# Kernel tuning notes

Measured on AMD Instinct MI355X. Metric: run time of the kernel, lower is better.

Reference implementation:

```python
import jax, jax.numpy as jnp
import numpy as np

DIM = 192; D_STATE = 16; D_CONV = 4; EXPAND = 2
D_INNER = EXPAND * DIM          # 384
DT_RANK = -(-DIM // 16)         # ceil(192/16) = 12
BSZ, T, H, W = 1, 16, 64, 64


def setup_inputs() -> dict:
    key = jax.random.key(0)
    ks = jax.random.split(key, 10)
    s = 0.02
    return {
        "x": jax.random.normal(ks[0], (BSZ, DIM, T, H, W), jnp.float32),
        "ln1_g": jnp.ones((DIM,), jnp.float32),
        "ln1_b": jnp.zeros((DIM,), jnp.float32),
        "ln2_g": jnp.ones((DIM,), jnp.float32),
        "ln2_b": jnp.zeros((DIM,), jnp.float32),
        "W_in": jax.random.normal(ks[1], (2 * D_INNER, DIM), jnp.float32) * s,
        "conv_w": jax.random.normal(ks[2], (D_INNER, D_CONV), jnp.float32) * 0.3,
        "conv_b": jnp.zeros((D_INNER,), jnp.float32),
        "W_xp": jax.random.normal(ks[3], (DT_RANK + 2 * D_STATE, D_INNER), jnp.float32) * s,
        "W_dt": jax.random.normal(ks[4], (D_INNER, DT_RANK), jnp.float32) * 0.1,
        "b_dt": jax.random.normal(ks[5], (D_INNER,), jnp.float32) * 0.1 - 4.0,
        "A_log": jnp.log(jnp.broadcast_to(jnp.arange(1, D_STATE + 1, dtype=jnp.float32), (D_INNER, D_STATE))),
        "D": jnp.ones((D_INNER,), jnp.float32),
        "W_out": jax.random.normal(ks[6], (DIM, D_INNER), jnp.float32) * s,
    }


def _layer_norm(x, g, b, eps=1e-5):
    m = x.mean(-1, keepdims=True)
    v = ((x - m) ** 2).mean(-1, keepdims=True)
    return (x - m) * jax.lax.rsqrt(v + eps) * g + b


def _mamba(tokens, W_in, conv_w, conv_b, W_xp, W_dt, b_dt, A_log, D, W_out):
    B, L, _ = tokens.shape
    xz = tokens @ W_in.T                      # (B, L, 2*d_inner)
    xc, z = jnp.split(xz, 2, axis=-1)
    # causal depthwise conv1d along L
    xin = xc.transpose(0, 2, 1)               # (B, d_inner, L)
    xconv = jax.lax.conv_general_dilated(
        xin, conv_w[:, None, :], (1,), [(D_CONV - 1, 0)],
        dimension_numbers=("NCH", "OIH", "NCH"), feature_group_count=D_INNER)
    xconv = xconv + conv_b[None, :, None]
    xs = jax.nn.silu(xconv.transpose(0, 2, 1))  # (B, L, d_inner)
    x_dbl = xs @ W_xp.T                        # (B, L, dt_rank + 2*d_state)
    dt, Bm, Cm = jnp.split(x_dbl, [DT_RANK, DT_RANK + D_STATE], axis=-1)
    dt = jax.nn.softplus(dt @ W_dt.T + b_dt)   # (B, L, d_inner)
    A = -jnp.exp(A_log)                        # (d_inner, d_state)
    dA = jnp.exp(dt[..., None] * A)            # (B, L, d_inner, d_state)
    dBx = dt[..., None] * Bm[:, :, None, :] * xs[..., None]

    def step(h, inp):
        dA_t, dBx_t, C_t = inp
        h = dA_t * h + dBx_t                   # (B, d_inner, d_state)
        return h, jnp.einsum("bds,bs->bd", h, C_t)

    h0 = jnp.zeros((B, D_INNER, D_STATE), tokens.dtype)
    _, ys = jax.lax.scan(step, h0, (dA.transpose(1, 0, 2, 3),
                                    dBx.transpose(1, 0, 2, 3),
                                    Cm.transpose(1, 0, 2)))
    y = ys.transpose(1, 0, 2) + xs * D         # (B, L, d_inner)
    y = y * jax.nn.silu(z)
    return y @ W_out.T                          # (B, L, dim)


def reference(x, ln1_g, ln1_b, ln2_g, ln2_b, W_in, conv_w, conv_b,
              W_xp, W_dt, b_dt, A_log, D, W_out):
    B, C, T_, H_, W_ = x.shape
    Hs, Ws = H_ // 4, W_ // 4
    # avg_pool3d kernel=(1,4,4) stride=(1,4,4)
    x_ds = x.reshape(B, C, T_, Hs, 4, Ws, 4).mean((4, 6))
    tokens = x_ds.reshape(B, C, T_ * Hs * Ws).transpose(0, 2, 1)  # (B, L, C)
    y = _layer_norm(tokens, ln1_g, ln1_b)
    y = _mamba(y, W_in, conv_w, conv_b, W_xp, W_dt, b_dt, A_log, D, W_out)
    out = _layer_norm(tokens + y, ln2_g, ln2_b)                    # (B, L, C)
    out5 = out.transpose(0, 2, 1).reshape(B, C, T_, Hs, Ws)
    pooled = out5.mean((3, 4))                                     # (B, C, T)
    mag = jnp.abs(jnp.fft.rfft(pooled, axis=2))
    weight = jax.nn.sigmoid(mag[:, :, 1:8].mean(-1))               # (B, C)
    out5 = out5 * weight[:, :, None, None, None]
    up = jax.image.resize(out5, (B, C, T_, H_, W_), method="trilinear")
    return up * jax.nn.sigmoid(x)
```

## Files before the change

### kernel.cpp

```cpp
#include <hip/hip_runtime.h>
#include <math.h>

#define DIMC 192
#define DI   384
#define DS   16
#define LTOK 4096
#define NCH  256
#define CLEN 16
#define NLANE (DI*DS)
#define L2E  1.4426950408889634f
#define LN2  0.6931471805599453f

typedef __attribute__((ext_vector_type(8))) short    bf16x8;
typedef __attribute__((ext_vector_type(8))) unsigned short u16x8;
typedef __attribute__((ext_vector_type(4))) float    f32x4;

__device__ __forceinline__ float EXP2(float x) { return __builtin_amdgcn_exp2f(x); }
__device__ __forceinline__ float RCP(float x)  { return __builtin_amdgcn_rcpf(x); }
__device__ __forceinline__ float LOG2(float x) { return __builtin_amdgcn_logf(x); }

__device__ __forceinline__ float sigmoidf_(float x) { return RCP(1.f + EXP2(-x * L2E)); }
__device__ __forceinline__ float siluf_(float x)    { return x * RCP(1.f + EXP2(-x * L2E)); }
__device__ __forceinline__ unsigned short f2bf(float f) {
    unsigned int u = __float_as_uint(f);
    u += 0x7FFFu + ((u >> 16) & 1u);
    return (unsigned short)(u >> 16);
}
__device__ __forceinline__ float bf2f(unsigned short b) {
    return __uint_as_float(((unsigned int)b) << 16);
}

__global__ __launch_bounds__(256) void poolln_kernel(const float* __restrict__ x,
                                                     const float* __restrict__ g,
                                                     const float* __restrict__ bb,
                                                     const float* __restrict__ W_in,
                                                     const float* __restrict__ W_out,
                                                     const float* __restrict__ W_xp,
                                                     const float* __restrict__ A_log,
                                                     float* __restrict__ tokens,
                                                     unsigned short* __restrict__ ytok,
                                                     unsigned short* __restrict__ W_in_bf,
                                                     unsigned short* __restrict__ W_out_bf,
                                                     unsigned short* __restrict__ W_xp_pad,
                                                     float* __restrict__ A2pre) {
    int blk = blockIdx.x;
    int tid = threadIdx.x;
    if (blk >= 256) {
        int id = (blk - 256) * 256 + tid;
        for (int i = id; i < 768 * 192; i += 8192) W_in_bf[i] = f2bf(W_in[i]);
        for (int i = id; i < 192 * 384; i += 8192) W_out_bf[i] = f2bf(W_out[i]);
        for (int i = id; i < 64 * 384; i += 8192) {
            int row = i / 384;
            W_xp_pad[i] = (row < 44) ? f2bf(W_xp[i]) : (unsigned short)0;
        }
        for (int i = id; i < NLANE; i += 8192) A2pre[i] = -expf(A_log[i]) * L2E;
        return;
    }
    int t = blk >> 4, hs = blk & 15;
    int grp = tid >> 4, ws = tid & 15;
    __shared__ float P[16 * 196];
    __shared__ float ms[16], rs[16];
    #pragma unroll
    for (int k = 0; k < 12; ++k) {
        int c = grp + (k << 4);
        const float* base = x + ((size_t)(c * 16 + t) * 64 + hs * 4) * 64 + ws * 4;
        float s = 0.f;
        #pragma unroll
        for (int i = 0; i < 4; ++i) {
            float4 v = *(const float4*)(base + i * 64);
            s += v.x + v.y + v.z + v.w;
        }
        P[ws * 196 + c] = s * 0.0625f;
    }
    __syncthreads();
    float s1 = 0.f, s2 = 0.f;
    #pragma unroll
    for (int k = 0; k < 12; ++k) {
        float v = P[grp * 196 + ws + 16 * k];
        s1 += v; s2 += v * v;
    }
    s1 += __shfl_xor(s1, 1); s2 += __shfl_xor(s2, 1);
    s1 += __shfl_xor(s1, 2); s2 += __shfl_xor(s2, 2);
    s1 += __shfl_xor(s1, 4); s2 += __shfl_xor(s2, 4);
    s1 += __shfl_xor(s1, 8); s2 += __shfl_xor(s2, 8);
    if (ws == 0) {
        float m = s1 * (1.f / 192.f);
        ms[grp] = m;
        rs[grp] = rsqrtf(s2 * (1.f / 192.f) - m * m + 1e-5f);
    }
    __syncthreads();
    int l0 = t * 256 + hs * 16;
    for (int e = tid; e < 16 * 192; e += 256) {
        int w2 = e / 192, c = e - w2 * 192;
        float v = P[w2 * 196 + c];
        float val = (v - ms[w2]) * rs[w2] * g[c] + bb[c];
        tokens[(size_t)(l0 + w2) * DIMC + c] = v;
        ytok[(size_t)(l0 + w2) * DIMC + c] = f2bf(val);
    }
}

template<int K>
__global__ __launch_bounds__(256) void gemm_mfma(const unsigned short* __restrict__ A,
                                                 const unsigned short* __restrict__ Wb,
                                                 float* __restrict__ Cout,
                                                 int N) {
    constexpr int KT = 192;
    constexpr int KP = KT + 8;
    __shared__ unsigned short As[64 * KP];
    __shared__ unsigned short Bs[64 * KP];
    int bm = blockIdx.y * 64;
    int bn = blockIdx.x * 64;
    int tid = threadIdx.x;
    int lane = tid & 63, w = tid >> 6;
    int wr = w >> 1, wc = w & 1;
    int r16 = lane & 15, h = lane >> 4;
    f32x4 acc[2][2] = {};
    for (int kt = 0; kt < K; kt += KT) {
        for (int c = tid; c < 64 * (KT / 8); c += 256) {
            int row = c / (KT / 8), col = (c % (KT / 8)) * 8;
            *(u16x8*)&As[row * KP + col] = *(const u16x8*)(A + (size_t)(bm + row) * K + kt + col);
            *(u16x8*)&Bs[row * KP + col] = *(const u16x8*)(Wb + (size_t)(bn + row) * K + kt + col);
        }
        __syncthreads();
        #pragma unroll
        for (int k0 = 0; k0 < KT; k0 += 32) {
            bf16x8 a0 = *(const bf16x8*)&As[(wr * 32 + r16)      * KP + k0 + 8 * h];
            bf16x8 a1 = *(const bf16x8*)&As[(wr * 32 + 16 + r16) * KP + k0 + 8 * h];
            bf16x8 b0 = *(const bf16x8*)&Bs[(wc * 32 + r16)      * KP + k0 + 8 * h];
            bf16x8 b1 = *(const bf16x8*)&Bs[(wc * 32 + 16 + r16) * KP + k0 + 8 * h];
            acc[0][0] = __builtin_amdgcn_mfma_f32_16x16x32_bf16(a0, b0, acc[0][0], 0, 0, 0);
            acc[0][1] = __builtin_amdgcn_mfma_f32_16x16x32_bf16(a0, b1, acc[0][1], 0, 0, 0);
            acc[1][0] = __builtin_amdgcn_mfma_f32_16x16x32_bf16(a1, b0, acc[1][0], 0, 0, 0);
            acc[1][1] = __builtin_amdgcn_mfma_f32_16x16x32_bf16(a1, b1, acc[1][1], 0, 0, 0);
        }
        __syncthreads();
    }
    #pragma unroll
    for (int fm = 0; fm < 2; ++fm)
        #pragma unroll
        for (int fn = 0; fn < 2; ++fn)
            #pragma unroll
            for (int i = 0; i < 4; ++i) {
                int r = bm + wr * 32 + fm * 16 + h * 4 + i;
                int cc = bn + wc * 32 + fn * 16 + r16;
                Cout[(size_t)r * N + cc] = acc[fm][fn][i];
            }
}

__global__ __launch_bounds__(256) void convxdbl(const float* __restrict__ xz,
                                                const float* __restrict__ conv_w,
                                                const float* __restrict__ conv_b,
                                                const unsigned short* __restrict__ Wxp,
                                                unsigned short* __restrict__ xsb,
                                                float* __restrict__ x_dbl) {
    int l0 = blockIdx.x * 16;
    int tid = threadIdx.x;
    __shared__ unsigned short As[16 * 392];
    __shared__ float xd[16 * 64];
    for (int e = tid * 2; e < 16 * 384; e += 512) {
        int row = e / 384, d = e - row * 384;
        int l = l0 + row;
        float ax = conv_b[d], ay = conv_b[d + 1];
        #pragma unroll
        for (int k = 0; k < 4; ++k) {
            int ll = l - 3 + k;
            if (ll >= 0) {
                float2 v = *(const float2*)(xz + (size_t)ll * 768 + d);
                ax = fmaf(conv_w[d * 4 + k],       v.x, ax);
                ay = fmaf(conv_w[(d + 1) * 4 + k], v.y, ay);
            }
        }
        ushort2 b2;
        b2.x = f2bf(siluf_(ax));
        b2.y = f2bf(siluf_(ay));
        *(ushort2*)&As[row * 392 + d] = b2;
        *(ushort2*)(xsb + (size_t)l * 384 + d) = b2;
    }
    __syncthreads();
    int lane = tid & 63, w = tid >> 6;
    int r16 = lane & 15, hh = lane >> 4;
    f32x4 acc = {};
    #pragma unroll
    for (int k0 = 0; k0 < 384; k0 += 32) {
        bf16x8 a = *(const bf16x8*)&As[r16 * 392 + k0 + 8 * hh];
        bf16x8 b = *(const bf16x8*)(Wxp + (size_t)(w * 16 + r16) * 384 + k0 + 8 * hh);
        acc = __builtin_amdgcn_mfma_f32_16x16x32_bf16(a, b, acc, 0, 0, 0);
    }
    #pragma unroll
    for (int i = 0; i < 4; ++i) xd[(hh * 4 + i) * 64 + w * 16 + r16] = acc[i];
    __syncthreads();
    {
        int e = tid * 4;
        int row = e >> 6, col = e & 63;
        *(float4*)(x_dbl + (size_t)(l0 + row) * 64 + col) = *(const float4*)&xd[e];
    }
}

__global__ __launch_bounds__(256) void scan1(const float* __restrict__ x_dbl,
                                             const unsigned short* __restrict__ xsb,
                                             const float* __restrict__ W_dt,
                                             const float* __restrict__ b_dt,
                                             const float* __restrict__ A2pre,
                                             float* __restrict__ chA,
                                             float* __restrict__ chB,
                                             float* __restrict__ Dloc,
                                             unsigned short* __restrict__ yloc) {
    int tid = threadIdx.x;
    int dg = blockIdx.x;
    int c  = blockIdx.y;
    __shared__ float xdblS[16 * 48];
    __shared__ float wdtS[64 * 13];
    __shared__ float dtS[16][64];
    __shared__ unsigned short xsS[16][64];
    for (int i = tid; i < 768; i += 256) {
        int row = i / 48, col = i - row * 48;
        xdblS[i] = x_dbl[(size_t)(c * 16 + row) * 64 + col];
    }
    for (int i = tid; i < 768; i += 256) {
        int dl_ = i / 12, r = i - dl_ * 12;
        wdtS[dl_ * 13 + r] = W_dt[(size_t)dg * 768 + i];
    }
    for (int i = tid; i < 1024; i += 256) {
        int row = i >> 6, dl_ = i & 63;
        xsS[row][dl_] = xsb[(size_t)(c * 16 + row) * 384 + dg * 64 + dl_];
    }
    __syncthreads();
    {
        int dl_ = tid & 63;
        float bd = b_dt[dg * 64 + dl_];
        #pragma unroll
        for (int i2 = 0; i2 < 4; ++i2) {
            int row = (tid >> 6) + 4 * i2;
            float s = bd;
            #pragma unroll
            for (int r = 0; r < 12; ++r)
                s = fmaf(xdblS[row * 48 + r], wdtS[dl_ * 13 + r], s);
            dtS[row][dl_] = (s > 20.f) ? s : LOG2(1.f + EXP2(s * L2E)) * LN2;
        }
    }
    __syncthreads();
    int sq = tid & 3, dl = tid >> 2;
    int d = dg * 64 + dl;
    float4 a4 = *(const float4*)(A2pre + (size_t)d * DS + sq * 4);
    float A2[4] = {a4.x, a4.y, a4.z, a4.w};
    float h[4] = {};
    float dts = 0.f;
    #pragma unroll
    for (int i = 0; i < CLEN; ++i) {
        int l = c * CLEN + i;
        float dtv = dtS[i][dl];
        float xv  = bf2f(xsS[i][dl]);
        float dtx = dtv * xv;
        dts += dtv;
        float y = 0.f;
        #pragma unroll
        for (int u = 0; u < 4; ++u) {
            float a = EXP2(dtv * A2[u]);
            h[u] = fmaf(a, h[u], dtx * xdblS[i * 48 + 12 + sq * 4 + u]);
            y = fmaf(h[u], xdblS[i * 48 + 28 + sq * 4 + u], y);
        }
        y += __shfl_xor(y, 1);
        y += __shfl_xor(y, 2);
        if (sq == 0) {
            yloc[(size_t)l * DI + d] = f2bf(y);
            Dloc[(size_t)l * DI + d] = dts;
        }
    }
    size_t base = (size_t)c * NLANE + d * DS + sq * 4;
    float4 pa, pb;
    pa.x = EXP2(dts * A2[0]); pa.y = EXP2(dts * A2[1]);
    pa.z = EXP2(dts * A2[2]); pa.w = EXP2(dts * A2[3]);
    pb.x = h[0]; pb.y = h[1]; pb.z = h[2]; pb.w = h[3];
    *(float4*)&chA[base] = pa;
    *(float4*)&chB[base] = pb;
}

__global__ __launch_bounds__(256) void scan2p(const float* __restrict__ chA,
                                              const float* __restrict__ chB,
                                              float* __restrict__ hst) {
    int tid = threadIdx.x;
    int ll = tid & 15;
    int g  = tid >> 4;
    int lane = blockIdx.x * 16 + ll;
    float a[16], b[16];
    #pragma unroll
    for (int i = 0; i < 16; ++i) {
        int c = g * 16 + i;
        a[i] = chA[(size_t)c * NLANE + lane];
        b[i] = chB[(size_t)c * NLANE + lane];
    }
    float Ath = 1.f, Bth = 0.f;
    #pragma unroll
    for (int i = 0; i < 16; ++i) {
        Bth = fmaf(a[i], Bth, b[i]);
        Ath *= a[i];
    }
    __shared__ float sA[16][17], sB[16][17];
    sA[g][ll] = Ath; sB[g][ll] = Bth;
    __syncthreads();
    #pragma unroll
    for (int step = 1; step < 16; step <<= 1) {
        float pA = 1.f, pB = 0.f;
        if (g >= step) { pA = sA[g - step][ll]; pB = sB[g - step][ll]; }
        __syncthreads();
        if (g >= step) {
            float cA = sA[g][ll], cB = sB[g][ll];
            sA[g][ll] = cA * pA;
            sB[g][ll] = fmaf(cA, pB, cB);
        }
        __syncthreads();
    }
    float h = (g == 0) ? 0.f : sB[g - 1][ll];
    #pragma unroll
    for (int i = 0; i < 16; ++i) {
        int c = g * 16 + i;
        hst[(size_t)c * NLANE + lane] = h;
        h = fmaf(a[i], h, b[i]);
    }
}

__global__ __launch_bounds__(256) void scan3fix(const float* __restrict__ hst,
                                                const float* __restrict__ Dloc,
                                                const float* __restrict__ x_dbl,
                                                const float* __restrict__ A2pre,
                                                const unsigned short* __restrict__ xsb,
                                                const float* __restrict__ xz,
                                                const float* __restrict__ Dvec,
                                                unsigned short* __restrict__ ybuf) {
    int dg = blockIdx.x;
    int c  = blockIdx.y;
    int tid = threadIdx.x;
    int ll = tid >> 4, dl = tid & 15;
    int d = dg * 16 + dl;
    int l = c * 16 + ll;
    __shared__ float hpS[16][17];
    __shared__ float A2S[16][17];
    __shared__ float CsS[256];
    {
        int dd = tid >> 4, ss = tid & 15;
        hpS[dd][ss] = hst[(size_t)c * NLANE + dg * 256 + tid];
        A2S[dd][ss] = A2pre[(size_t)dg * 256 + tid];
        CsS[tid]    = x_dbl[(size_t)(c * 16 + dd) * 64 + 28 + ss];
    }
    __syncthreads();
    float Dl = Dloc[(size_t)l * DI + d];
    float y  = bf2f(ybuf[(size_t)l * DI + d]);
    float xv = bf2f(xsb[(size_t)l * DI + d]);
    float z  = xz[(size_t)l * 768 + 384 + d];
    #pragma unroll
    for (int s = 0; s < 16; ++s) {
        float e = EXP2(A2S[dl][s] * Dl);
        y = fmaf(CsS[ll * 16 + s] * e, hpS[dl][s], y);
    }
    float val = (y + xv * Dvec[d]) * siluf_(z);
    ybuf[(size_t)l * DI + d] = f2bf(val);
}

__global__ __launch_bounds__(256) void gemmln(const unsigned short* __restrict__ A,
                                              const unsigned short* __restrict__ Wb,
                                              const float* __restrict__ tokens,
                                              const float* __restrict__ g,
                                              const float* __restrict__ bb,
                                              float* __restrict__ o5) {
    constexpr int K = 384, KT = 96, KP = KT + 8;
    __shared__ unsigned short As[16 * KP];
    __shared__ unsigned short Bs[192 * KP];
    __shared__ float P[16 * 193];
    __shared__ float ms[16], rs[16];
    int bm = blockIdx.x * 16;
    int tid = threadIdx.x;
    int lane = tid & 63, w = tid >> 6;
    int r16 = lane & 15, hh = lane >> 4;
    f32x4 acc[3] = {};
    for (int kt = 0; kt < K; kt += KT) {
        if (tid < 192) {
            int row = tid / 12, col = (tid % 12) * 8;
            *(u16x8*)&As[row * KP + col] = *(const u16x8*)(A + (size_t)(bm + row) * K + kt + col);
        }
        for (int cc = tid; cc < 192 * 12; cc += 256) {
            int row = cc / 12, col = (cc % 12) * 8;
            *(u16x8*)&Bs[row * KP + col] = *(const u16x8*)(Wb + (size_t)row * K + kt + col);
        }
        __syncthreads();
        #pragma unroll
        for (int k0 = 0; k0 < KT; k0 += 32) {
            bf16x8 a = *(const bf16x8*)&As[r16 * KP + k0 + 8 * hh];
            #pragma unroll
            for (int j = 0; j < 3; ++j) {
                bf16x8 b = *(const bf16x8*)&Bs[((w * 3 + j) * 16 + r16) * KP + k0 + 8 * hh];
                acc[j] = __builtin_amdgcn_mfma_f32_16x16x32_bf16(a, b, acc[j], 0, 0, 0);
            }
        }
        __syncthreads();
    }
    for (int e = tid; e < 16 * 192; e += 256) {
        int row = e / 192, col = e - row * 192;
        P[row * 193 + col] = tokens[(size_t)(bm + row) * DIMC + col];
    }
    __syncthreads();
    #pragma unroll
    for (int j = 0; j < 3; ++j)
        #pragma unroll
        for (int i = 0; i < 4; ++i)
            P[(hh * 4 + i) * 193 + (w * 3 + j) * 16 + r16] += acc[j][i];
    __syncthreads();
    {
        int tk = tid >> 4, q = tid & 15;
        float s1 = 0.f, s2 = 0.f;
        #pragma unroll
        for (int u = 0; u < 12; ++u) {
            float v = P[tk * 193 + q * 12 + u];
            s1 += v; s2 += v * v;
        }
        s1 += __shfl_xor(s1, 1); s2 += __shfl_xor(s2, 1);
        s1 += __shfl_xor(s1, 2); s2 += __shfl_xor(s2, 2);
        s1 += __shfl_xor(s1, 4); s2 += __shfl_xor(s2, 4);
        s1 += __shfl_xor(s1, 8); s2 += __shfl_xor(s2, 8);
        if (q == 0) {
            float m = s1 * (1.f / 192.f);
            ms[tk] = m;
            rs[tk] = rsqrtf(s2 * (1.f / 192.f) - m * m + 1e-5f);
        }
    }
    __syncthreads();
    int t = bm >> 8;
    int sp0 = bm & 255;
    for (int e = tid; e < 16 * 192; e += 256) {
        int cch = e >> 4, row = e & 15;
        float val = (P[row * 193 + cch] - ms[row]) * rs[row] * g[cch] + bb[cch];
        o5[(size_t)cch * 4096 + t * 256 + sp0 + row] = val;
    }
}

__global__ __launch_bounds__(256) void upfft(const float* __restrict__ o5,
                                             const float* __restrict__ x,
                                             float* __restrict__ out) {
    int blk = blockIdx.x;
    int c = blk >> 4, t = blk & 15;
    int tid = threadIdx.x;
    __shared__ float pl[256];
    __shared__ float pooled[16];
    __shared__ float mag[8];
    __shared__ float wgt_s;
    int wv = tid >> 6, lane = tid & 63;
    #pragma unroll
    for (int rr = 0; rr < 4; ++rr) {
        int r = wv * 4 + rr;
        float s = 0.f;
        #pragma unroll
        for (int u = 0; u < 4; ++u) {
            float v = o5[(size_t)c * 4096 + r * 256 + lane + u * 64];
            s += v;
            if (r == t) pl[lane + u * 64] = v;
        }
        s += __shfl_xor(s, 1); s += __shfl_xor(s, 2); s += __shfl_xor(s, 4);
        s += __shfl_xor(s, 8); s += __shfl_xor(s, 16); s += __shfl_xor(s, 32);
        if (lane == 0) pooled[r] = s * (1.f / 256.f);
    }
    __syncthreads();
    if (tid >= 1 && tid <= 7) {
        int k = tid;
        float re = 0.f, im = 0.f;
        for (int tt = 0; tt < 16; ++tt) {
            float ang = -0.39269908169872414f * (float)(k * tt);
            re = fmaf(pooled[tt], cosf(ang), re);
            im = fmaf(pooled[tt], sinf(ang), im);
        }
        mag[k] = sqrtf(re * re + im * im);
    }
    __syncthreads();
    if (tid == 0) {
        float m = 0.f;
        for (int k = 1; k <= 7; ++k) m += mag[k];
        wgt_s = sigmoidf_(m * (1.f / 7.f));
    }
    __syncthreads();
    float wc = wgt_s;
    size_t planeoff = (size_t)blk * 4096;
    #pragma unroll
    for (int p = 0; p < 4; ++p) {
        int px4 = p * 256 + tid;
        int k = px4 & 15;
        int hrow = px4 >> 4;
        float sh = hrow * 0.25f - 0.375f;
        int h0 = (int)floorf(sh); float fh = sh - (float)h0;
        int h0c = min(max(h0, 0), 15), h1c = min(max(h0 + 1, 0), 15);
        int cm = max(k - 1, 0), cp = min(k + 1, 15);
        float r0m = pl[h0c * 16 + cm], r00 = pl[h0c * 16 + k], r0p = pl[h0c * 16 + cp];
        float r1m = pl[h1c * 16 + cm], r10 = pl[h1c * 16 + k], r1p = pl[h1c * 16 + cp];
        float gh = 1.f - fh;
        float vm = r0m * gh + r1m * fh;
        float v0 = r00 * gh + r10 * fh;
        float vp = r0p * gh + r1p * fh;
        size_t off = planeoff + (size_t)px4 * 4;
        float4 xv = *(const float4*)(x + off);
        float4 o;
        o.x = (vm * 0.375f + v0 * 0.625f) * wc * sigmoidf_(xv.x);
        o.y = (vm * 0.125f + v0 * 0.875f) * wc * sigmoidf_(xv.y);
        o.z = (v0 * 0.875f + vp * 0.125f) * wc * sigmoidf_(xv.z);
        o.w = (v0 * 0.625f + vp * 0.375f) * wc * sigmoidf_(xv.w);
        *(float4*)(out + off) = o;
    }
}

extern "C" void kernel_launch(void* const* d_in, const int* in_sizes, int n_in,
                              void* d_out, int out_size, void* d_ws, size_t ws_size,
                              hipStream_t stream) {
    const float* x      = (const float*)d_in[0];
    const float* ln1_g  = (const float*)d_in[1];
    const float* ln1_b  = (const float*)d_in[2];
    const float* ln2_g  = (const float*)d_in[3];
    const float* ln2_b  = (const float*)d_in[4];
    const float* W_in   = (const float*)d_in[5];
    const float* conv_w = (const float*)d_in[6];
    const float* conv_b = (const float*)d_in[7];
    const float* W_xp   = (const float*)d_in[8];
    const float* W_dt   = (const float*)d_in[9];
    const float* b_dt   = (const float*)d_in[10];
    const float* A_log  = (const float*)d_in[11];
    const float* Dvec   = (const float*)d_in[12];
    const float* W_out  = (const float*)d_in[13];
    float* out = (float*)d_out;

    float* ws = (float*)d_ws;
    float* tokens = ws;  ws += (size_t)LTOK * DIMC;
    float* xz     = ws;  ws += (size_t)LTOK * 768;
    float* x_dbl  = ws;  ws += (size_t)LTOK * 64;
    float* chA    = ws;  ws += (size_t)NLANE * NCH;
    float* chB    = ws;  ws += (size_t)NLANE * NCH;
    float* hst    = ws;  ws += (size_t)NLANE * NCH;
    float* Dloc   = ws;  ws += (size_t)LTOK * DI;
    float* o5     = ws;  ws += (size_t)DIMC * LTOK;
    float* A2pre  = ws;  ws += NLANE;
    unsigned short* ytok     = (unsigned short*)ws;  ws += (size_t)LTOK * DIMC / 2;
    unsigned short* ybuf     = (unsigned short*)ws;  ws += (size_t)LTOK * DI / 2;
    unsigned short* xsb      = (unsigned short*)ws;  ws += (size_t)LTOK * DI / 2;
    unsigned short* W_in_bf  = (unsigned short*)ws;  ws += (size_t)768 * 192 / 2;
    unsigned short* W_out_bf = (unsigned short*)ws;  ws += (size_t)192 * 384 / 2;
    unsigned short* W_xp_pad = (unsigned short*)ws;  ws += (size_t)64 * 384 / 2;

    poolln_kernel<<<288, 256, 0, stream>>>(x, ln1_g, ln1_b, W_in, W_out, W_xp, A_log,
                                           tokens, ytok, W_in_bf, W_out_bf, W_xp_pad, A2pre);
    gemm_mfma<192><<<dim3(12, 64), 256, 0, stream>>>(ytok, W_in_bf, xz, 768);
    convxdbl<<<256, 256, 0, stream>>>(xz, conv_w, conv_b, W_xp_pad, xsb, x_dbl);
    scan1<<<dim3(6, NCH), 256, 0, stream>>>(x_dbl, xsb, W_dt, b_dt, A2pre, chA, chB, Dloc, ybuf);
    scan2p<<<NLANE / 16, 256, 0, stream>>>(chA, chB, hst);
    scan3fix<<<dim3(24, NCH), 256, 0, stream>>>(hst, Dloc, x_dbl, A2pre, xsb, xz, Dvec, ybuf);
    gemmln<<<256, 256, 0, stream>>>(ybuf, W_out_bf, tokens, ln2_g, ln2_b, o5);
    upfft<<<3072, 256, 0, stream>>>(o5, x, out);
}
```

Before: 125.5 us.

## Fuse scan fix-up into output GEMM+LN and emit bf16 x/silu(z) from input GEMM

The input projection GEMM now writes bf16 xc and a precomputed bf16 silu(z) instead of a float32 xz buffer, which halves that intermediate traffic. The scan fix-up kernel is merged into the W_out GEMM + LayerNorm kernel (512 threads per 16-token chunk), so the gated y stays in shared memory and is never written to or read back from global memory. This drops one launch but gives the fused kernel only 256 blocks, each doing serial work over 12 d-groups. It also switches the FFT to fast __sinf/__cosf, and storing z and xc in bf16 adds some rounding.

New measurement: 110.9 us. 1.13x faster.

```diff
diff --git a/kernel.cpp b/kernel.cpp
--- a/kernel.cpp
+++ b/kernel.cpp
@@ -99,13 +99,11 @@
     }
 }
 
-template<int K>
-__global__ __launch_bounds__(256) void gemm_mfma(const unsigned short* __restrict__ A,
-                                                 const unsigned short* __restrict__ Wb,
-                                                 float* __restrict__ Cout,
-                                                 int N) {
-    constexpr int KT = 192;
-    constexpr int KP = KT + 8;
+__global__ __launch_bounds__(256) void gemm_in(const unsigned short* __restrict__ A,
+                                               const unsigned short* __restrict__ Wb,
+                                               unsigned short* __restrict__ xcb,
+                                               unsigned short* __restrict__ zsb) {
+    constexpr int K = 192, KP = K + 8;
     __shared__ unsigned short As[64 * KP];
     __shared__ unsigned short Bs[64 * KP];
     int bm = blockIdx.y * 64;
@@ -114,27 +112,25 @@
     int lane = tid & 63, w = tid >> 6;
     int wr = w >> 1, wc = w & 1;
     int r16 = lane & 15, h = lane >> 4;
+    for (int c = tid; c < 64 * (K / 8); c += 256) {
+        int row = c / (K / 8), col = (c % (K / 8)) * 8;
+        *(u16x8*)&As[row * KP + col] = *(const u16x8*)(A + (size_t)(bm + row) * K + col);
+        *(u16x8*)&Bs[row * KP + col] = *(const u16x8*)(Wb + (size_t)(bn + row) * K + col);
+    }
+    __syncthreads();
     f32x4 acc[2][2] = {};
-    for (int kt = 0; kt < K; kt += KT) {
-        for (int c = tid; c < 64 * (KT / 8); c += 256) {
-            int row = c / (KT / 8), col = (c % (KT / 8)) * 8;
-            *(u16x8*)&As[row * KP + col] = *(const u16x8*)(A + (size_t)(bm + row) * K + kt + col);
-            *(u16x8*)&Bs[row * KP + col] = *(const u16x8*)(Wb + (size_t)(bn + row) * K + kt + col);
-        }
-        __syncthreads();
-        #pragma unroll
-        for (int k0 = 0; k0 < KT; k0 += 32) {
-            bf16x8 a0 = *(const bf16x8*)&As[(wr * 32 + r16)      * KP + k0 + 8 * h];
-            bf16x8 a1 = *(const bf16x8*)&As[(wr * 32 + 16 + r16) * KP + k0 + 8 * h];
-            bf16x8 b0 = *(const bf16x8*)&Bs[(wc * 32 + r16)      * KP + k0 + 8 * h];
-            bf16x8 b1 = *(const bf16x8*)&Bs[(wc * 32 + 16 + r16) * KP + k0 + 8 * h];
-            acc[0][0] = __builtin_amdgcn_mfma_f32_16x16x32_bf16(a0, b0, acc[0][0], 0, 0, 0);
-            acc[0][1] = __builtin_amdgcn_mfma_f32_16x16x32_bf16(a0, b1, acc[0][1], 0, 0, 0);
-            acc[1][0] = __builtin_amdgcn_mfma_f32_16x16x32_bf16(a1, b0, acc[1][0], 0, 0, 0);
-            acc[1][1] = __builtin_amdgcn_mfma_f32_16x16x32_bf16(a1, b1, acc[1][1], 0, 0, 0);
-        }
-        __syncthreads();
-    }
+    #pragma unroll
+    for (int k0 = 0; k0 < K; k0 += 32) {
+        bf16x8 a0 = *(const bf16x8*)&As[(wr * 32 + r16)      * KP + k0 + 8 * h];
+        bf16x8 a1 = *(const bf16x8*)&As[(wr * 32 + 16 + r16) * KP + k0 + 8 * h];
+        bf16x8 b0 = *(const bf16x8*)&Bs[(wc * 32 + r16)      * KP + k0 + 8 * h];
+        bf16x8 b1 = *(const bf16x8*)&Bs[(wc * 32 + 16 + r16) * KP + k0 + 8 * h];
+        acc[0][0] = __builtin_amdgcn_mfma_f32_16x16x32_bf16(a0, b0, acc[0][0], 0, 0, 0);
+        acc[0][1] = __builtin_amdgcn_mfma_f32_16x16x32_bf16(a0, b1, acc[0][1], 0, 0, 0);
+        acc[1][0] = __builtin_amdgcn_mfma_f32_16x16x32_bf16(a1, b0, acc[1][0], 0, 0, 0);
+        acc[1][1] = __builtin_amdgcn_mfma_f32_16x16x32_bf16(a1, b1, acc[1][1], 0, 0, 0);
+    }
+    bool isz = (bn >= 384);
     #pragma unroll
     for (int fm = 0; fm < 2; ++fm)
         #pragma unroll
@@ -143,11 +139,13 @@
             for (int i = 0; i < 4; ++i) {
                 int r = bm + wr * 32 + fm * 16 + h * 4 + i;
                 int cc = bn + wc * 32 + fn * 16 + r16;
-                Cout[(size_t)r * N + cc] = acc[fm][fn][i];
+                float v = acc[fm][fn][i];
+                if (isz) zsb[(size_t)r * DI + (cc - 384)] = f2bf(siluf_(v));
+                else     xcb[(size_t)r * DI + cc]         = f2bf(v);
             }
 }
 
-__global__ __launch_bounds__(256) void convxdbl(const float* __restrict__ xz,
+__global__ __launch_bounds__(256) void convxdbl(const unsigned short* __restrict__ xcb,
                                                 const float* __restrict__ conv_w,
                                                 const float* __restrict__ conv_b,
                                                 const unsigned short* __restrict__ Wxp,
@@ -165,9 +163,9 @@
         for (int k = 0; k < 4; ++k) {
             int ll = l - 3 + k;
             if (ll >= 0) {
-                float2 v = *(const float2*)(xz + (size_t)ll * 768 + d);
-                ax = fmaf(conv_w[d * 4 + k],       v.x, ax);
-                ay = fmaf(conv_w[(d + 1) * 4 + k], v.y, ay);
+                ushort2 u = *(const ushort2*)(xcb + (size_t)ll * DI + d);
+                ax = fmaf(conv_w[d * 4 + k],       bf2f(u.x), ax);
+                ay = fmaf(conv_w[(d + 1) * 4 + k], bf2f(u.y), ay);
             }
         }
         ushort2 b2;
@@ -319,103 +317,100 @@
     }
 }
 
-__global__ __launch_bounds__(256) void scan3fix(const float* __restrict__ hst,
-                                                const float* __restrict__ Dloc,
-                                                const float* __restrict__ x_dbl,
-                                                const float* __restrict__ A2pre,
-                                                const unsigned short* __restrict__ xsb,
-                                                const float* __restrict__ xz,
-                                                const float* __restrict__ Dvec,
-                                                unsigned short* __restrict__ ybuf) {
-    int dg = blockIdx.x;
-    int c  = blockIdx.y;
-    int tid = threadIdx.x;
-    int ll = tid >> 4, dl = tid & 15;
-    int d = dg * 16 + dl;
+__global__ __launch_bounds__(512) void gemmscanln(const float* __restrict__ hst,
+                                                  const float* __restrict__ Dloc,
+                                                  const float* __restrict__ x_dbl,
+                                                  const float* __restrict__ A2pre,
+                                                  const unsigned short* __restrict__ yloc,
+                                                  const unsigned short* __restrict__ xsb,
+                                                  const unsigned short* __restrict__ zsb,
+                                                  const float* __restrict__ Dvec,
+                                                  const unsigned short* __restrict__ Wb,
+                                                  const float* __restrict__ tokens,
+                                                  const float* __restrict__ g,
+                                                  const float* __restrict__ bb,
+                                                  float* __restrict__ o5) {
+    constexpr int K = 384, KT = 96, KP = KT + 8;
+    __shared__ unsigned short ybufS[16 * 392];
+    __shared__ char smem2[192 * KP * 2];
+    unsigned short* Bs = (unsigned short*)smem2;
+    float* P = (float*)smem2;
+    __shared__ float hpS[2][16 * 17];
+    __shared__ float A2S[2][16 * 17];
+    __shared__ float CsS[256];
+    __shared__ float ms[16], rs[16];
+    int c = blockIdx.x;
+    int tid = threadIdx.x;
+    int half = tid >> 8, t8 = tid & 255;
+    int ll = t8 >> 4, sl = t8 & 15;
+    if (tid < 256) CsS[tid] = x_dbl[(size_t)(c * 16 + (tid >> 4)) * 64 + 28 + (tid & 15)];
     int l = c * 16 + ll;
-    __shared__ float hpS[16][17];
-    __shared__ float A2S[16][17];
-    __shared__ float CsS[256];
-    {
-        int dd = tid >> 4, ss = tid & 15;
-        hpS[dd][ss] = hst[(size_t)c * NLANE + dg * 256 + tid];
-        A2S[dd][ss] = A2pre[(size_t)dg * 256 + tid];
-        CsS[tid]    = x_dbl[(size_t)(c * 16 + dd) * 64 + 28 + ss];
-    }
-    __syncthreads();
-    float Dl = Dloc[(size_t)l * DI + d];
-    float y  = bf2f(ybuf[(size_t)l * DI + d]);
-    float xv = bf2f(xsb[(size_t)l * DI + d]);
-    float z  = xz[(size_t)l * 768 + 384 + d];
-    #pragma unroll
-    for (int s = 0; s < 16; ++s) {
-        float e = EXP2(A2S[dl][s] * Dl);
-        y = fmaf(CsS[ll * 16 + s] * e, hpS[dl][s], y);
-    }
-    float val = (y + xv * Dvec[d]) * siluf_(z);
-    ybuf[(size_t)l * DI + d] = f2bf(val);
-}
-
-__global__ __launch_bounds__(256) void gemmln(const unsigned short* __restrict__ A,
-                                              const unsigned short* __restrict__ Wb,
-                                              const float* __restrict__ tokens,
-                                              const float* __restrict__ g,
-                                              const float* __restrict__ bb,
-                                              float* __restrict__ o5) {
-    constexpr int K = 384, KT = 96, KP = KT + 8;
-    __shared__ unsigned short As[16 * KP];
-    __shared__ unsigned short Bs[192 * KP];
-    __shared__ float P[16 * 193];
-    __shared__ float ms[16], rs[16];
-    int bm = blockIdx.x * 16;
-    int tid = threadIdx.x;
+    for (int dgi = 0; dgi < 12; ++dgi) {
+        int dg = dgi * 2 + half;
+        hpS[half][ll * 17 + sl] = hst[(size_t)c * NLANE + dg * 256 + t8];
+        A2S[half][ll * 17 + sl] = A2pre[(size_t)dg * 256 + t8];
+        __syncthreads();
+        int d = dg * 16 + sl;
+        float Dl = Dloc[(size_t)l * DI + d];
+        float y  = bf2f(yloc[(size_t)l * DI + d]);
+        float xv = bf2f(xsb[(size_t)l * DI + d]);
+        float zs = bf2f(zsb[(size_t)l * DI + d]);
+        #pragma unroll
+        for (int s = 0; s < 16; ++s) {
+            float e = EXP2(A2S[half][sl * 17 + s] * Dl);
+            y = fmaf(CsS[ll * 16 + s] * e, hpS[half][sl * 17 + s], y);
+        }
+        float val = (y + xv * Dvec[d]) * zs;
+        ybufS[ll * 392 + d] = f2bf(val);
+        __syncthreads();
+    }
     int lane = tid & 63, w = tid >> 6;
     int r16 = lane & 15, hh = lane >> 4;
-    f32x4 acc[3] = {};
+    f32x4 acc0 = {}, acc1 = {};
     for (int kt = 0; kt < K; kt += KT) {
-        if (tid < 192) {
-            int row = tid / 12, col = (tid % 12) * 8;
-            *(u16x8*)&As[row * KP + col] = *(const u16x8*)(A + (size_t)(bm + row) * K + kt + col);
-        }
-        for (int cc = tid; cc < 192 * 12; cc += 256) {
-            int row = cc / 12, col = (cc % 12) * 8;
+        for (int cc2 = tid; cc2 < 192 * 12; cc2 += 512) {
+            int row = cc2 / 12, col = (cc2 % 12) * 8;
             *(u16x8*)&Bs[row * KP + col] = *(const u16x8*)(Wb + (size_t)row * K + kt + col);
         }
         __syncthreads();
         #pragma unroll
         for (int k0 = 0; k0 < KT; k0 += 32) {
-            bf16x8 a = *(const bf16x8*)&As[r16 * KP + k0 + 8 * hh];
-            #pragma unroll
-            for (int j = 0; j < 3; ++j) {
-                bf16x8 b = *(const bf16x8*)&Bs[((w * 3 + j) * 16 + r16) * KP + k0 + 8 * hh];
-                acc[j] = __builtin_amdgcn_mfma_f32_16x16x32_bf16(a, b, acc[j], 0, 0, 0);
+            bf16x8 a = *(const bf16x8*)&ybufS[r16 * 392 + kt + k0 + 8 * hh];
+            bf16x8 b0 = *(const bf16x8*)&Bs[(w * 16 + r16) * KP + k0 + 8 * hh];
+            acc0 = __builtin_amdgcn_mfma_f32_16x16x32_bf16(a, b0, acc0, 0, 0, 0);
+            if (w < 4) {
+                bf16x8 b1 = *(const bf16x8*)&Bs[((8 + w) * 16 + r16) * KP + k0 + 8 * hh];
+                acc1 = __builtin_amdgcn_mfma_f32_16x16x32_bf16(a, b1, acc1, 0, 0, 0);
             }
         }
         __syncthreads();
     }
-    for (int e = tid; e < 16 * 192; e += 256) {
+    for (int e = tid; e < 16 * 192; e += 512) {
         int row = e / 192, col = e - row * 192;
-        P[row * 193 + col] = tokens[(size_t)(bm + row) * DIMC + col];
-    }
-    __syncthreads();
-    #pragma unroll
-    for (int j = 0; j < 3; ++j)
+        P[row * 193 + col] = tokens[(size_t)(c * 16 + row) * DIMC + col];
+    }
+    __syncthreads();
+    #pragma unroll
+    for (int i = 0; i < 4; ++i)
+        P[(hh * 4 + i) * 193 + w * 16 + r16] += acc0[i];
+    if (w < 4)
         #pragma unroll
         for (int i = 0; i < 4; ++i)
-            P[(hh * 4 + i) * 193 + (w * 3 + j) * 16 + r16] += acc[j][i];
+            P[(hh * 4 + i) * 193 + (8 + w) * 16 + r16] += acc1[i];
     __syncthreads();
     {
-        int tk = tid >> 4, q = tid & 15;
+        int tk = tid >> 5, q = tid & 31;
         float s1 = 0.f, s2 = 0.f;
         #pragma unroll
-        for (int u = 0; u < 12; ++u) {
-            float v = P[tk * 193 + q * 12 + u];
+        for (int u = 0; u < 6; ++u) {
+            float v = P[tk * 193 + q * 6 + u];
             s1 += v; s2 += v * v;
         }
-        s1 += __shfl_xor(s1, 1); s2 += __shfl_xor(s2, 1);
-        s1 += __shfl_xor(s1, 2); s2 += __shfl_xor(s2, 2);
-        s1 += __shfl_xor(s1, 4); s2 += __shfl_xor(s2, 4);
-        s1 += __shfl_xor(s1, 8); s2 += __shfl_xor(s2, 8);
+        s1 += __shfl_xor(s1, 1);  s2 += __shfl_xor(s2, 1);
+        s1 += __shfl_xor(s1, 2);  s2 += __shfl_xor(s2, 2);
+        s1 += __shfl_xor(s1, 4);  s2 += __shfl_xor(s2, 4);
+        s1 += __shfl_xor(s1, 8);  s2 += __shfl_xor(s2, 8);
+        s1 += __shfl_xor(s1, 16); s2 += __shfl_xor(s2, 16);
         if (q == 0) {
             float m = s1 * (1.f / 192.f);
             ms[tk] = m;
@@ -423,9 +418,9 @@
         }
     }
     __syncthreads();
-    int t = bm >> 8;
-    int sp0 = bm & 255;
-    for (int e = tid; e < 16 * 192; e += 256) {
+    int t = c >> 4;
+    int sp0 = (c * 16) & 255;
+    for (int e = tid; e < 16 * 192; e += 512) {
         int cch = e >> 4, row = e & 15;
         float val = (P[row * 193 + cch] - ms[row]) * rs[row] * g[cch] + bb[cch];
         o5[(size_t)cch * 4096 + t * 256 + sp0 + row] = val;
@@ -463,8 +458,8 @@
         float re = 0.f, im = 0.f;
         for (int tt = 0; tt < 16; ++tt) {
             float ang = -0.39269908169872414f * (float)(k * tt);
-            re = fmaf(pooled[tt], cosf(ang), re);
-            im = fmaf(pooled[tt], sinf(ang), im);
+            re = fmaf(pooled[tt], __cosf(ang), re);
+            im = fmaf(pooled[tt], __sinf(ang), im);
         }
         mag[k] = sqrtf(re * re + im * im);
     }
@@ -524,7 +519,6 @@
 
     float* ws = (float*)d_ws;
     float* tokens = ws;  ws += (size_t)LTOK * DIMC;
-    float* xz     = ws;  ws += (size_t)LTOK * 768;
     float* x_dbl  = ws;  ws += (size_t)LTOK * 64;
     float* chA    = ws;  ws += (size_t)NLANE * NCH;
     float* chB    = ws;  ws += (size_t)NLANE * NCH;
@@ -533,19 +527,21 @@
     float* o5     = ws;  ws += (size_t)DIMC * LTOK;
     float* A2pre  = ws;  ws += NLANE;
     unsigned short* ytok     = (unsigned short*)ws;  ws += (size_t)LTOK * DIMC / 2;
-    unsigned short* ybuf     = (unsigned short*)ws;  ws += (size_t)LTOK * DI / 2;
+    unsigned short* yloc     = (unsigned short*)ws;  ws += (size_t)LTOK * DI / 2;
     unsigned short* xsb      = (unsigned short*)ws;  ws += (size_t)LTOK * DI / 2;
+    unsigned short* xcb      = (unsigned short*)ws;  ws += (size_t)LTOK * DI / 2;
+    unsigned short* zsb      = (unsigned short*)ws;  ws += (size_t)LTOK * DI / 2;
     unsigned short* W_in_bf  = (unsigned short*)ws;  ws += (size_t)768 * 192 / 2;
     unsigned short* W_out_bf = (unsigned short*)ws;  ws += (size_t)192 * 384 / 2;
     unsigned short* W_xp_pad = (unsigned short*)ws;  ws += (size_t)64 * 384 / 2;
 
     poolln_kernel<<<288, 256, 0, stream>>>(x, ln1_g, ln1_b, W_in, W_out, W_xp, A_log,
                                            tokens, ytok, W_in_bf, W_out_bf, W_xp_pad, A2pre);
-    gemm_mfma<192><<<dim3(12, 64), 256, 0, stream>>>(ytok, W_in_bf, xz, 768);
-    convxdbl<<<256, 256, 0, stream>>>(xz, conv_w, conv_b, W_xp_pad, xsb, x_dbl);
-    scan1<<<dim3(6, NCH), 256, 0, stream>>>(x_dbl, xsb, W_dt, b_dt, A2pre, chA, chB, Dloc, ybuf);
+    gemm_in<<<dim3(12, 64), 256, 0, stream>>>(ytok, W_in_bf, xcb, zsb);
+    convxdbl<<<256, 256, 0, stream>>>(xcb, conv_w, conv_b, W_xp_pad, xsb, x_dbl);
+    scan1<<<dim3(6, NCH), 256, 0, stream>>>(x_dbl, xsb, W_dt, b_dt, A2pre, chA, chB, Dloc, yloc);
     scan2p<<<NLANE / 16, 256, 0, stream>>>(chA, chB, hst);
-    scan3fix<<<dim3(24, NCH), 256, 0, stream>>>(hst, Dloc, x_dbl, A2pre, xsb, xz, Dvec, ybuf);
-    gemmln<<<256, 256, 0, stream>>>(ybuf, W_out_bf, tokens, ln2_g, ln2_b, o5);
+    gemmscanln<<<256, 512, 0, stream>>>(hst, Dloc, x_dbl, A2pre, yloc, xsb, zsb, Dvec,
+                                        W_out_bf, tokens, ln2_g, ln2_b, o5);
     upfft<<<3072, 256, 0, stream>>>(o5, x, out);
 }
```
